# Optimization experiments

Measured on AMD Instinct MI355X. Metric: run time of the kernel, lower is better.

## Reference

```python
import jax, jax.numpy as jnp
import numpy as np

CHANNELS = 512
NUM_HEADS = 4
GROUPS = 32
EPS = 1e-5


def setup_inputs() -> dict:
    key = jax.random.key(0)
    ks = jax.random.split(key, 7)
    C = CHANNELS
    x = jax.random.normal(ks[0], (16, C, 32, 32), dtype=jnp.float32)
    norm_w = jnp.ones((C,), dtype=jnp.float32)
    norm_b = jnp.zeros((C,), dtype=jnp.float32)
    qkv_w = jax.random.normal(ks[1], (3 * C, C), dtype=jnp.float32) * (C ** -0.5)
    qkv_b = jnp.zeros((3 * C,), dtype=jnp.float32)
    proj_w = jax.random.normal(ks[2], (C, C), dtype=jnp.float32) * (C ** -0.5)
    proj_b = jnp.zeros((C,), dtype=jnp.float32)
    return {"x": x, "norm_w": norm_w, "norm_b": norm_b,
            "qkv_w": qkv_w, "qkv_b": qkv_b,
            "proj_w": proj_w, "proj_b": proj_b}


def reference(x, norm_w, norm_b, qkv_w, qkv_b, proj_w, proj_b):
    B, C, H, W = x.shape
    heads = NUM_HEADS
    hd = C // heads  # head dim
    N = H * W

    # GroupNorm(32, C): normalize over (C/32, H, W) per group, then per-channel affine
    xg = x.reshape(B, GROUPS, -1)
    mu = jnp.mean(xg, axis=-1, keepdims=True)
    var = jnp.var(xg, axis=-1, keepdims=True)
    h = ((xg - mu) * jax.lax.rsqrt(var + EPS)).reshape(B, C, H, W)
    h = h * norm_w[None, :, None, None] + norm_b[None, :, None, None]

    # 1x1 conv qkv: [B,C,H,W] -> [B,3C,H,W]
    qkv = jnp.einsum('oc,bchw->bohw', qkv_w, h) + qkv_b[None, :, None, None]
    qkv = qkv.reshape(B, 3, heads, hd, N)
    q, k, v = qkv[:, 0], qkv[:, 1], qkv[:, 2]  # each [B, heads, hd, N]

    scale = hd ** -0.5
    attn = jnp.einsum('bhcn,bhcm->bhnm', q, k) * scale  # [B, heads, N, N]
    attn = jax.nn.softmax(attn, axis=-1)
    h = jnp.einsum('bhnm,bhcm->bhcn', attn, v).reshape(B, C, H, W)

    # 1x1 conv proj + residual
    h = jnp.einsum('oc,bchw->bohw', proj_w, h) + proj_b[None, :, None, None]
    return x + h
```

## Files before the change

kernel.cpp:

```cpp
#include <hip/hip_runtime.h>

typedef __bf16 v8bf __attribute__((ext_vector_type(8)));
typedef float  v4f  __attribute__((ext_vector_type(4)));
typedef unsigned short u16;

__device__ __forceinline__ u16 f2bf(float f){
  __bf16 h = (__bf16)f;
  union { __bf16 h; u16 u; } c; c.h = h; return c.u;
}
__device__ __forceinline__ v4f v4zero(){ v4f z; z[0]=0.f; z[1]=0.f; z[2]=0.f; z[3]=0.f; return z; }

#define MFMA16(a,b,c) __builtin_amdgcn_mfma_f32_16x16x32_bf16((a),(b),(c),0,0,0)

__device__ __forceinline__ void gl_lds16(const u16* g, u16* l){
  __builtin_amdgcn_global_load_lds((const __attribute__((address_space(1))) void*)g,
                                   (__attribute__((address_space(3))) void*)l, 16, 0, 0);
}

__global__ __launch_bounds__(256) void cvt_kernel(const float* __restrict__ src, u16* __restrict__ dst, int n){
  int i = (blockIdx.x*256 + threadIdx.x)*4;
  if (i < n){
    float4 v = *(const float4*)(src + i);
    ushort4 o;
    o.x = f2bf(v.x); o.y = f2bf(v.y); o.z = f2bf(v.z); o.w = f2bf(v.w);
    *(ushort4*)(dst + i) = o;
  }
}

__global__ __launch_bounds__(256) void gn_stats_kernel(const float* __restrict__ x, float* __restrict__ stats){
  const float* base = x + (size_t)blockIdx.x * 16384;
  float s = 0.f, ss = 0.f;
  #pragma unroll
  for (int it = 0; it < 16; ++it){
    float4 v = *(const float4*)(base + it*1024 + threadIdx.x*4);
    s  += v.x + v.y + v.z + v.w;
    ss += v.x*v.x + v.y*v.y + v.z*v.z + v.w*v.w;
  }
  #pragma unroll
  for (int off = 32; off > 0; off >>= 1){ s += __shfl_down(s, off); ss += __shfl_down(ss, off); }
  __shared__ float red[8];
  int w = threadIdx.x >> 6;
  if ((threadIdx.x & 63) == 0){ red[w] = s; red[4+w] = ss; }
  __syncthreads();
  if (threadIdx.x == 0){
    float S  = red[0]+red[1]+red[2]+red[3];
    float SS = red[4]+red[5]+red[6]+red[7];
    float mean = S * (1.f/16384.f);
    float var  = SS * (1.f/16384.f) - mean*mean;
    stats[blockIdx.x*2]   = mean;
    stats[blockIdx.x*2+1] = rsqrtf(var + 1e-5f);
  }
}

__global__ __launch_bounds__(256) void gn_apply_kernel(const float* __restrict__ x, const float* __restrict__ nw,
                                                       const float* __restrict__ nb, const float* __restrict__ stats,
                                                       u16* __restrict__ h_t){
  __shared__ u16 tile[32*520];
  int b = blockIdx.y, n0 = blockIdx.x*32, tid = threadIdx.x;
  int cr = tid >> 2, nn = (tid & 3)*8;
  #pragma unroll
  for (int p = 0; p < 8; ++p){
    int c = p*64 + cr;
    const float* px = x + (size_t)(b*512 + c)*1024 + n0 + nn;
    float4 u0 = *(const float4*)(px);
    float4 u1 = *(const float4*)(px + 4);
    int g = c >> 4;
    float mean = stats[(b*32+g)*2], rstd = stats[(b*32+g)*2+1];
    float wv = nw[c], bv = nb[c];
    float vals[8] = {u0.x,u0.y,u0.z,u0.w,u1.x,u1.y,u1.z,u1.w};
    #pragma unroll
    for (int e = 0; e < 8; ++e)
      tile[(nn+e)*520 + c] = f2bf((vals[e] - mean)*rstd*wv + bv);
  }
  __syncthreads();
  #pragma unroll
  for (int p = 0; p < 8; ++p){
    int n  = p*4 + (tid >> 6);
    int c0 = (tid & 63)*8;
    *(int4*)(h_t + ((size_t)b*1024 + n0 + n)*512 + c0) = *(int4*)(tile + n*520 + c0);
  }
}

__global__ __launch_bounds__(256,2) void gemm_bt_kernel(
    const u16* __restrict__ A, long long sA,
    const u16* __restrict__ B, long long sB,
    u16* __restrict__ Cbf, float* __restrict__ Cf, long long sC,
    const float* __restrict__ bias_row,
    const float* __restrict__ bias_col,
    const float* __restrict__ residf, long long sR,
    int M, int N, int K)
{
  __shared__ u16 smem[18432];
  u16* As = smem;
  u16* Bs = smem + 128*64;
  const int tid = threadIdx.x, w = tid>>6, lane = tid&63, col = lane&15, quad = lane>>4;
  const int m0 = blockIdx.y*128, n0 = blockIdx.x*128;
  const int lr8 = lane>>3;
  const int gsw = ((lane&7) ^ lr8)*8;
  const u16* Ag = A + (size_t)blockIdx.z*sA + (size_t)(m0 + w*32 + lr8)*K + gsw;
  const u16* Bg = B + (size_t)blockIdx.z*sB + (size_t)(n0 + w*32 + lr8)*K + gsw;
  u16* ldsA = As + (w*32)*64;
  u16* ldsB = Bs + (w*32)*64;
  const int mw = (w&1)*64, nw = (w>>1)*64;
  const int csw = col&7;

  v4f acc[4][4];
  #pragma unroll
  for (int i=0;i<4;++i)
    #pragma unroll
    for (int j=0;j<4;++j) acc[i][j] = v4zero();

  for (int kt = 0; kt < K; kt += 64){
    #pragma unroll
    for (int p = 0; p < 4; ++p){
      gl_lds16(Ag + (size_t)(p*8)*K + kt, ldsA + p*512);
      gl_lds16(Bg + (size_t)(p*8)*K + kt, ldsB + p*512);
    }
    __syncthreads();
    #pragma unroll
    for (int kh = 0; kh < 2; ++kh){
      const int fs = ((kh*4 + quad) ^ csw)*8;
      v8bf a[4], bb[4];
      #pragma unroll
      for (int i = 0; i < 4; ++i) a[i]  = *(const v8bf*)(As + (mw+i*16+col)*64 + fs);
      #pragma unroll
      for (int j = 0; j < 4; ++j) bb[j] = *(const v8bf*)(Bs + (nw+j*16+col)*64 + fs);
      #pragma unroll
      for (int i = 0; i < 4; ++i)
        #pragma unroll
        for (int j = 0; j < 4; ++j)
          acc[i][j] = MFMA16(a[i], bb[j], acc[i][j]);
    }
    __syncthreads();
  }

  float br[4][4], bc[4];
  #pragma unroll
  for (int i = 0; i < 4; ++i)
    #pragma unroll
    for (int r = 0; r < 4; ++r)
      br[i][r] = bias_row ? bias_row[m0+mw+i*16+quad*4+r] : 0.f;
  #pragma unroll
  for (int j = 0; j < 4; ++j)
    bc[j] = bias_col ? bias_col[n0+nw+j*16+col] : 0.f;

  if (Cf){
    float* Cb = Cf + (size_t)blockIdx.z*sC;
    const float* Rb = residf ? residf + (size_t)blockIdx.z*sR : nullptr;
    #pragma unroll
    for (int i = 0; i < 4; ++i)
      #pragma unroll
      for (int r = 0; r < 4; ++r){
        int row = m0+mw+i*16+quad*4+r;
        #pragma unroll
        for (int j = 0; j < 4; ++j){
          size_t goff = (size_t)row*N + n0+nw+j*16+col;
          float val = acc[i][j][r] + br[i][r] + bc[j];
          if (Rb) val += Rb[goff];
          Cb[goff] = val;
        }
      }
  } else {
    u16* Cs = smem + w*(64*72);
    #pragma unroll
    for (int i = 0; i < 4; ++i)
      #pragma unroll
      for (int j = 0; j < 4; ++j)
        #pragma unroll
        for (int r = 0; r < 4; ++r)
          Cs[(i*16+quad*4+r)*72 + j*16+col] = f2bf(acc[i][j][r] + br[i][r] + bc[j]);
    __syncthreads();
    u16* Cb = Cbf + (size_t)blockIdx.z*sC;
    #pragma unroll
    for (int p = 0; p < 8; ++p){
      int rl = p*8 + (lane>>3), cl = (lane&7)*8;
      size_t goff = (size_t)(m0+mw+rl)*N + n0+nw+cl;
      *(int4*)(Cb + goff) = *(int4*)(Cs + rl*72 + cl);
    }
  }
}

__global__ __launch_bounds__(256,2) void attn_kernel(const u16* __restrict__ qk, const u16* __restrict__ vv,
                                                     u16* __restrict__ outp){
  __shared__ u16 smem[25600];
  u16* Ks = smem;
  u16* Vs = smem + 8192;
  u16* Ps = smem + 8192 + 9216;
  const int id = blockIdx.x;
  const int qt = id >> 6, bh = id & 63, b = bh >> 2, h = bh & 3;
  const int n0 = qt*128;
  const int tid = threadIdx.x, w = tid>>6, lane = tid&63, col = lane&15, quad = lane>>4;
  const size_t bq = (size_t)b*1024*1024;
  const float scale2 = 0.12751742f;

  if (tid < 128){
    int r = 128 + (tid>>3);
    int pat = (r == 128) ? (int)0x3F803F80u : 0;
    int4 v; v.x = pat; v.y = pat; v.z = pat; v.w = pat;
    *(int4*)(Vs + r*64 + (tid&7)*8) = v;
  }

  v8bf aq[2][4];
  #pragma unroll
  for (int i = 0; i < 2; ++i)
    #pragma unroll
    for (int kk = 0; kk < 4; ++kk)
      aq[i][kk] = *(const v8bf*)(qk + bq + (size_t)(n0 + w*32 + i*16 + col)*1024 + h*128 + kk*32 + quad*8);

  v4f o[2][9];
  #pragma unroll
  for (int i=0;i<2;++i)
    #pragma unroll
    for (int j=0;j<9;++j) o[i][j] = v4zero();

  const int krow = w*4 + (lane>>4);
  const int kgr  = (lane&15) ^ (krow&7);
  const u16* kg_base = qk + bq + (size_t)krow*1024 + 512 + h*128 + kgr*8;
  u16* kl_base = Ks + (w*4)*128;
  const int vrow = w*8 + (lane>>3);
  const int vgr  = (lane&7) ^ (vrow&7);
  const u16* vg_base = vv + ((size_t)b*512 + h*128 + vrow)*1024 + vgr*8;
  u16* vl_base = Vs + (w*8)*64;

  for (int mt = 0; mt < 1024; mt += 64){
    #pragma unroll
    for (int p = 0; p < 4; ++p)
      gl_lds16(kg_base + (size_t)(mt + p*16)*1024, kl_base + p*16*128);
    #pragma unroll
    for (int p = 0; p < 4; ++p)
      gl_lds16(vg_base + (size_t)(p*32)*1024 + mt, vl_base + p*32*64);
    __syncthreads();

    v4f s[2][4];
    #pragma unroll
    for (int i=0;i<2;++i)
      #pragma unroll
      for (int j=0;j<4;++j) s[i][j] = v4zero();
    #pragma unroll
    for (int kk = 0; kk < 4; ++kk){
      v8bf bk[4];
      #pragma unroll
      for (int j = 0; j < 4; ++j){
        int r = j*16 + col;
        int g = (kk*4 + quad) ^ (r&7);
        bk[j] = *(const v8bf*)(Ks + (r<<7) + (g<<3));
      }
      #pragma unroll
      for (int i = 0; i < 2; ++i)
        #pragma unroll
        for (int j = 0; j < 4; ++j)
          s[i][j] = MFMA16(aq[i][kk], bk[j], s[i][j]);
    }

    #pragma unroll
    for (int i = 0; i < 2; ++i)
      #pragma unroll
      for (int j = 0; j < 4; ++j)
        #pragma unroll
        for (int r = 0; r < 4; ++r){
          int rr = w*32 + i*16 + quad*4 + r;
          int m  = j*16 + col;
          int key = (rr ^ (rr>>3)) & 7;
          Ps[(rr<<6) + ((((m>>3) ^ key))<<3) + (m&7)] = f2bf(exp2f(s[i][j][r]*scale2));
        }

    #pragma unroll
    for (int kk = 0; kk < 2; ++kk){
      v8bf ap[2];
      #pragma unroll
      for (int i = 0; i < 2; ++i){
        int rr = w*32 + i*16 + col;
        int key = (rr ^ (rr>>3)) & 7;
        int g = (kk*4 + quad) ^ key;
        ap[i] = *(const v8bf*)(Ps + (rr<<6) + (g<<3));
      }
      #pragma unroll
      for (int j = 0; j < 9; ++j){
        int vr = j*16 + col;
        int g = (kk*4 + quad) ^ (vr&7);
        v8bf bv = *(const v8bf*)(Vs + (vr<<6) + (g<<3));
        #pragma unroll
        for (int i = 0; i < 2; ++i) o[i][j] = MFMA16(ap[i], bv, o[i][j]);
      }
    }
    __syncthreads();
  }

  #pragma unroll
  for (int i = 0; i < 2; ++i)
    #pragma unroll
    for (int r = 0; r < 4; ++r){
      float l = __shfl(o[i][8][r], quad<<4);
      float inv = 1.f / l;
      #pragma unroll
      for (int j = 0; j < 8; ++j) o[i][j][r] *= inv;
    }

  #pragma unroll
  for (int i = 0; i < 2; ++i)
    #pragma unroll
    for (int j = 0; j < 8; ++j)
      #pragma unroll
      for (int r = 0; r < 4; ++r){
        int rr = w*32 + i*16 + quad*4 + r;
        int c  = j*16 + col;
        smem[(rr<<7) + ((((c>>3) ^ (rr&7))<<3)) + (c&7)] = f2bf(o[i][j][r]);
      }
  __syncthreads();
  #pragma unroll
  for (int p = 0; p < 8; ++p){
    int nr = p*16 + (tid>>4);
    int gc = (tid&15) ^ (nr&7);
    *(int4*)(outp + ((size_t)b*1024 + n0 + nr)*512 + h*128 + ((tid&15)<<3)) =
      *(int4*)(smem + (nr<<7) + (gc<<3));
  }
}

extern "C" void kernel_launch(void* const* d_in, const int* in_sizes, int n_in,
                              void* d_out, int out_size, void* d_ws, size_t ws_size,
                              hipStream_t stream){
  const float* x      = (const float*)d_in[0];
  const float* norm_w = (const float*)d_in[1];
  const float* norm_b = (const float*)d_in[2];
  const float* qkv_w  = (const float*)d_in[3];
  const float* qkv_b  = (const float*)d_in[4];
  const float* proj_w = (const float*)d_in[5];
  const float* proj_b = (const float*)d_in[6];
  float* out = (float*)d_out;

  u16* h_t   = (u16*)d_ws;
  u16* qk_t  = h_t  + (size_t)16*1024*512;
  u16* v_ws  = qk_t + (size_t)16*1024*1024;
  u16* wq_bf = v_ws + (size_t)16*512*1024;
  u16* wp_bf = wq_bf + (size_t)1536*512;
  float* stats = (float*)(wp_bf + (size_t)512*512);
  u16* attnout = h_t;

  cvt_kernel<<<768, 256, 0, stream>>>(qkv_w, wq_bf, 1536*512);
  cvt_kernel<<<256, 256, 0, stream>>>(proj_w, wp_bf, 512*512);
  gn_stats_kernel<<<512, 256, 0, stream>>>(x, stats);
  gn_apply_kernel<<<dim3(32,16), 256, 0, stream>>>(x, norm_w, norm_b, stats, h_t);

  gemm_bt_kernel<<<dim3(8,8,16), 256, 0, stream>>>(
      h_t, (long long)1024*512, wq_bf, 0,
      qk_t, nullptr, (long long)1024*1024, nullptr, qkv_b, nullptr, 0, 1024, 1024, 512);

  gemm_bt_kernel<<<dim3(8,4,16), 256, 0, stream>>>(
      wq_bf + (size_t)1024*512, 0, h_t, (long long)1024*512,
      v_ws, nullptr, (long long)512*1024, qkv_b + 1024, nullptr, nullptr, 0, 512, 1024, 512);

  attn_kernel<<<512, 256, 0, stream>>>(qk_t, v_ws, attnout);

  gemm_bt_kernel<<<dim3(8,4,16), 256, 0, stream>>>(
      wp_bf, 0, attnout, (long long)1024*512,
      nullptr, out, (long long)512*1024, proj_b, nullptr, x, (long long)512*1024, 512, 1024, 512);
}
```

Baseline: 221.3 us.

## Fuse QK and V projection GEMMs into one kernel with 128x256 tiles

Replaces the two separate QKV projection GEMM launches with a single kernel that computes h_t × Wqkv^T using 128x256 tiles. Blocks whose output columns fall in the Q/K range write row-major into qk_t, and blocks in the V range transpose their tile through LDS into v_ws. This removes one launch and lets V share the same A-operand layout instead of swapping operands. In exchange the larger tile uses more registers (a 4x8 accumulator array per warp) and more LDS, which may reduce occupancy.

```diff
diff --git a/kernel.cpp b/kernel.cpp
--- a/kernel.cpp
+++ b/kernel.cpp
@@ -78,6 +78,103 @@
     int n  = p*4 + (tid >> 6);
     int c0 = (tid & 63)*8;
     *(int4*)(h_t + ((size_t)b*1024 + n0 + n)*512 + c0) = *(int4*)(tile + n*520 + c0);
+  }
+}
+
+__global__ __launch_bounds__(256,2) void gemm_qkv_kernel(
+    const u16* __restrict__ A,
+    const u16* __restrict__ B,
+    const float* __restrict__ bias,
+    u16* __restrict__ qk_t, u16* __restrict__ v_ws)
+{
+  __shared__ u16 smem[24576];
+  u16* As = smem;
+  u16* Bs = smem + 128*64;
+  const int tid = threadIdx.x, w = tid>>6, lane = tid&63, col = lane&15, quad = lane>>4;
+  const int m0 = blockIdx.y*128;
+  const int n0 = blockIdx.x*256;
+  const int b  = blockIdx.z;
+  const int lr8 = lane>>3;
+  const int gsw = ((lane&7) ^ lr8)*8;
+  const u16* Ag = A + ((size_t)b*1024 + m0 + w*32 + lr8)*512 + gsw;
+  const u16* Bg = B + (size_t)(n0 + w*64 + lr8)*512 + gsw;
+  u16* ldsA = As + (w*32)*64;
+  u16* ldsB = Bs + (w*64)*64;
+  const int mw = (w&1)*64, nw = (w>>1)*128;
+  const int csw = col&7;
+
+  v4f acc[4][8];
+  #pragma unroll
+  for (int i=0;i<4;++i)
+    #pragma unroll
+    for (int j=0;j<8;++j) acc[i][j] = v4zero();
+
+  for (int kt = 0; kt < 512; kt += 64){
+    #pragma unroll
+    for (int p = 0; p < 4; ++p)
+      gl_lds16(Ag + (size_t)(p*8)*512 + kt, ldsA + p*512);
+    #pragma unroll
+    for (int p = 0; p < 8; ++p)
+      gl_lds16(Bg + (size_t)(p*8)*512 + kt, ldsB + p*512);
+    __syncthreads();
+    #pragma unroll
+    for (int kh = 0; kh < 2; ++kh){
+      const int fs = ((kh*4 + quad) ^ csw)*8;
+      v8bf a[4], bb[8];
+      #pragma unroll
+      for (int i = 0; i < 4; ++i) a[i]  = *(const v8bf*)(As + (mw+i*16+col)*64 + fs);
+      #pragma unroll
+      for (int j = 0; j < 8; ++j) bb[j] = *(const v8bf*)(Bs + (nw+j*16+col)*64 + fs);
+      #pragma unroll
+      for (int i = 0; i < 4; ++i)
+        #pragma unroll
+        for (int j = 0; j < 8; ++j)
+          acc[i][j] = MFMA16(a[i], bb[j], acc[i][j]);
+    }
+    __syncthreads();
+  }
+
+  float bc[8];
+  #pragma unroll
+  for (int j = 0; j < 8; ++j)
+    bc[j] = bias[n0 + nw + j*16 + col];
+
+  if (n0 < 1024){
+    u16* Cs = smem + w*(64*72);
+    #pragma unroll
+    for (int half = 0; half < 2; ++half){
+      #pragma unroll
+      for (int i = 0; i < 4; ++i)
+        #pragma unroll
+        for (int jj = 0; jj < 4; ++jj)
+          #pragma unroll
+          for (int r = 0; r < 4; ++r)
+            Cs[(i*16+quad*4+r)*72 + jj*16+col] = f2bf(acc[i][half*4+jj][r] + bc[half*4+jj]);
+      u16* dst = qk_t + (size_t)b*1024*1024;
+      #pragma unroll
+      for (int p = 0; p < 8; ++p){
+        int rl = p*8 + (lane>>3), cl = (lane&7)*8;
+        *(int4*)(dst + (size_t)(m0+mw+rl)*1024 + n0+nw+half*64+cl) = *(int4*)(Cs + rl*72 + cl);
+      }
+    }
+  } else {
+    u16* Ct = smem + w*(64*80);
+    #pragma unroll
+    for (int half = 0; half < 2; ++half){
+      #pragma unroll
+      for (int i = 0; i < 4; ++i)
+        #pragma unroll
+        for (int jj = 0; jj < 4; ++jj)
+          #pragma unroll
+          for (int r = 0; r < 4; ++r)
+            Ct[(jj*16+col)*80 + i*16+quad*4+r] = f2bf(acc[i][half*4+jj][r] + bc[half*4+jj]);
+      u16* dst = v_ws + (size_t)b*512*1024;
+      #pragma unroll
+      for (int p = 0; p < 8; ++p){
+        int rl = p*8 + (lane>>3), cl = (lane&7)*8;
+        *(int4*)(dst + (size_t)(n0-1024 + nw + half*64 + rl)*1024 + m0+mw+cl) = *(int4*)(Ct + rl*80 + cl);
+      }
+    }
   }
 }
 
@@ -341,13 +438,7 @@
   gn_stats_kernel<<<512, 256, 0, stream>>>(x, stats);
   gn_apply_kernel<<<dim3(32,16), 256, 0, stream>>>(x, norm_w, norm_b, stats, h_t);
 
-  gemm_bt_kernel<<<dim3(8,8,16), 256, 0, stream>>>(
-      h_t, (long long)1024*512, wq_bf, 0,
-      qk_t, nullptr, (long long)1024*1024, nullptr, qkv_b, nullptr, 0, 1024, 1024, 512);
-
-  gemm_bt_kernel<<<dim3(8,4,16), 256, 0, stream>>>(
-      wq_bf + (size_t)1024*512, 0, h_t, (long long)1024*512,
-      v_ws, nullptr, (long long)512*1024, qkv_b + 1024, nullptr, nullptr, 0, 512, 1024, 512);
+  gemm_qkv_kernel<<<dim3(6,8,16), 256, 0, stream>>>(h_t, wq_bf, qkv_b, qk_t, v_ws);
 
   attn_kernel<<<512, 256, 0, stream>>>(qk_t, v_ws, attnout);
 
```

Result: no change. 218.8 us (-1.1%).
